# Kernel optimization log

Measured on AMD Instinct MI355X. Metric: run time of the kernel, lower is better.

The kernel has to match this reference:

```python
import jax, jax.numpy as jnp
import numpy as np

NUM_USERS = 100000
NUM_ITEMS = 50000
NUM_OTHERS = 20000
N_NODES = NUM_USERS + NUM_ITEMS + NUM_OTHERS
LATENT_DIM = 64
N_LAYERS = 3
NNZ = 5000000
BATCH = 8192


def setup_inputs() -> dict:
    key = jax.random.key(0)
    ks = jax.random.split(key, 8)
    user_emb = jax.random.normal(ks[0], (NUM_USERS, LATENT_DIM), dtype=jnp.float32) * 0.1
    item_emb = jax.random.normal(ks[1], (NUM_ITEMS, LATENT_DIM), dtype=jnp.float32) * 0.1
    other_emb = jax.random.normal(ks[2], (NUM_OTHERS, LATENT_DIM), dtype=jnp.float32) * 0.1
    # normalized-adjacency-like positive values (symmetric norm values are small positives)
    vals = jax.random.uniform(ks[3], (NNZ,), dtype=jnp.float32) * 0.02
    row_idx = jax.random.randint(ks[4], (NNZ,), 0, N_NODES, dtype=jnp.int64 if jax.config.jax_enable_x64 else jnp.int32)
    col_idx = jax.random.randint(ks[5], (NNZ,), 0, N_NODES, dtype=jnp.int64 if jax.config.jax_enable_x64 else jnp.int32)
    users = jax.random.randint(ks[6], (BATCH,), 0, NUM_USERS, dtype=jnp.int32)
    items = jax.random.randint(ks[7], (BATCH,), 0, NUM_ITEMS, dtype=jnp.int32)
    return {
        "user_emb": user_emb,
        "item_emb": item_emb,
        "other_emb": other_emb,
        "vals": vals,
        "row_idx": row_idx,
        "col_idx": col_idx,
        "users": users,
        "items": items,
    }


def _spmm(vals, row_idx, col_idx, x):
    # sparse.mm(A, x): out[r] = sum_{(r,c) in A} vals * x[c]
    gathered = vals[:, None] * x[col_idx]  # [nnz, d]
    return jax.ops.segment_sum(gathered, row_idx, num_segments=N_NODES)


def reference(user_emb, item_emb, other_emb, vals, row_idx, col_idx, users, items):
    all_emb = jnp.concatenate([user_emb, item_emb, other_emb], axis=0)  # [N, d]
    acc = all_emb
    cur = all_emb
    for _ in range(N_LAYERS):
        cur = _spmm(vals, row_idx, col_idx, cur)
        acc = acc + cur
    lgn_out = acc / jnp.float32(N_LAYERS + 1)  # mean over stacked layer embeddings
    all_users = lgn_out[:NUM_USERS]
    all_items = lgn_out[NUM_USERS:NUM_USERS + NUM_ITEMS]
    users_embs = all_users[users]  # [B, d]
    items_embs = all_items[items]  # [B, d]
    gamma = jnp.sum(users_embs * items_embs, axis=1)  # [B]
    return gamma
```

## Files before the change

### kernel.cpp

```cpp
#include <hip/hip_runtime.h>

#define NUM_USERS 100000
#define NUM_ITEMS 50000
#define NUM_OTHERS 20000
#define N_NODES 170000
#define DIM 64
#define NNZ 5000000
#define BATCH 8192

#define BSHIFT 10
#define RPB (1 << BSHIFT)
#define NBUCK ((N_NODES + RPB - 1) / RPB)
#define COLMASK 0x3FFFF
#define NBLK 512
#define CHUNK ((NNZ + NBLK - 1) / NBLK)
#define HBLK 1024
#define HCHUNK ((NNZ + HBLK - 1) / HBLK)

typedef float f32x2 __attribute__((ext_vector_type(2)));

static __device__ __forceinline__ unsigned f2bf(float f) {
    unsigned u = __float_as_uint(f);
    u = (u + 0x7fff + ((u >> 16) & 1)) >> 16;
    return u;
}
static __device__ __forceinline__ float bflo(unsigned u) {
    return __uint_as_float(u << 16);
}
static __device__ __forceinline__ float bfhi(unsigned u) {
    return __uint_as_float(u & 0xFFFF0000u);
}

__global__ void build_cur0(const float* __restrict__ ue,
                           const float* __restrict__ ie,
                           const float* __restrict__ oe,
                           ushort4* __restrict__ cur) {
    const int total = N_NODES * (DIM / 4);
    for (int i = blockIdx.x * blockDim.x + threadIdx.x; i < total;
         i += gridDim.x * blockDim.x) {
        const int node = i >> 4;
        const int sub  = i & 15;
        const float* src;
        if (node < NUM_USERS)                  src = ue + (size_t)node * DIM;
        else if (node < NUM_USERS + NUM_ITEMS) src = ie + (size_t)(node - NUM_USERS) * DIM;
        else                                   src = oe + (size_t)(node - NUM_USERS - NUM_ITEMS) * DIM;
        const float4 f = reinterpret_cast<const float4*>(src)[sub];
        ushort4 o;
        o.x = (unsigned short)f2bf(f.x); o.y = (unsigned short)f2bf(f.y);
        o.z = (unsigned short)f2bf(f.z); o.w = (unsigned short)f2bf(f.w);
        cur[i] = o;
    }
}

__global__ void init_acc(const int* __restrict__ users,
                         const int* __restrict__ items,
                         const float* __restrict__ ue,
                         const float* __restrict__ ie,
                         float4* __restrict__ uacc,
                         float4* __restrict__ iacc) {
    const int total = BATCH * (DIM / 4);
    int i = blockIdx.x * blockDim.x + threadIdx.x;
    if (i >= total) return;
    const int b = i >> 4;
    const int sub = i & 15;
    uacc[i] = reinterpret_cast<const float4*>(ue + (size_t)users[b] * DIM)[sub];
    iacc[i] = reinterpret_cast<const float4*>(ie + (size_t)items[b] * DIM)[sub];
}

__global__ __launch_bounds__(256) void bucket_hist(const int* __restrict__ rows,
                                                   int* __restrict__ bucket_cnt) {
    __shared__ int h[NBUCK];
    for (int i = threadIdx.x; i < NBUCK; i += 256) h[i] = 0;
    __syncthreads();
    const int s = blockIdx.x * HCHUNK;
    const int e = min(s + HCHUNK, NNZ);
    for (int i = s + threadIdx.x; i < e; i += 256)
        atomicAdd(&h[rows[i] >> BSHIFT], 1);
    __syncthreads();
    for (int i = threadIdx.x; i < NBUCK; i += 256)
        if (h[i]) atomicAdd(&bucket_cnt[i], h[i]);
}

__global__ __launch_bounds__(256) void bucket_scan(const int* __restrict__ bucket_cnt,
                                                   int* __restrict__ bucket_base,
                                                   int* __restrict__ gcursor) {
    __shared__ int lds[256];
    const int t = threadIdx.x;
    const int v = (t < NBUCK) ? bucket_cnt[t] : 0;
    lds[t] = v;
    __syncthreads();
    int acc = v;
    for (int off = 1; off < 256; off <<= 1) {
        const int add = (t >= off) ? lds[t - off] : 0;
        __syncthreads();
        acc += add;
        lds[t] = acc;
        __syncthreads();
    }
    if (t < NBUCK) {
        const int ex = acc - v;
        bucket_base[t] = ex;
        gcursor[t] = ex;
    }
    if (t == 0) bucket_base[NBUCK] = NNZ;
}

__global__ __launch_bounds__(256) void bucket_scatter(const int* __restrict__ rows,
                                                      const int* __restrict__ cols,
                                                      const float* __restrict__ vals,
                                                      int* __restrict__ gcursor,
                                                      int2* __restrict__ bkt) {
    __shared__ int h[NBUCK];
    __shared__ int base[NBUCK];
    for (int i = threadIdx.x; i < NBUCK; i += 256) h[i] = 0;
    __syncthreads();
    const int s = blockIdx.x * CHUNK;
    const int e = min(s + CHUNK, NNZ);
    for (int i = s + threadIdx.x; i < e; i += 256)
        atomicAdd(&h[rows[i] >> BSHIFT], 1);
    __syncthreads();
    for (int i = threadIdx.x; i < NBUCK; i += 256)
        base[i] = h[i] ? atomicAdd(&gcursor[i], h[i]) : 0;
    __syncthreads();
    for (int i = threadIdx.x; i < NBUCK; i += 256) h[i] = 0;
    __syncthreads();
    for (int i = s + threadIdx.x; i < e; i += 256) {
        const int r  = rows[i];
        const int bk = r >> BSHIFT;
        const int lr = r & (RPB - 1);
        const int pos = base[bk] + atomicAdd(&h[bk], 1);
        bkt[pos] = make_int2((lr << 18) | cols[i], __float_as_int(vals[i]));
    }
}

__global__ __launch_bounds__(512) void bucket_to_csr(const int* __restrict__ bucket_base,
                                                     const int2* __restrict__ bkt,
                                                     unsigned* __restrict__ rowinfo,
                                                     int2* __restrict__ packed) {
    __shared__ int cnt[RPB];
    __shared__ int rs[RPB];
    __shared__ int tsum[512];
    const int k = blockIdx.x;
    const int rbase = k << BSHIFT;
    const int bs = bucket_base[k];
    const int be = bucket_base[k + 1];
    const int t = threadIdx.x;

    cnt[t] = 0; cnt[t + 512] = 0;
    __syncthreads();
    for (int i = bs + t; i < be; i += 512)
        atomicAdd(&cnt[bkt[i].x >> 18], 1);
    __syncthreads();

    const int v0 = cnt[2 * t];
    const int v1 = cnt[2 * t + 1];
    int acc = v0 + v1;
    tsum[t] = acc;
    __syncthreads();
    for (int off = 1; off < 512; off <<= 1) {
        const int add = (t >= off) ? tsum[t - off] : 0;
        __syncthreads();
        acc += add;
        tsum[t] = acc;
        __syncthreads();
    }
    const int excl = acc - (v0 + v1);
    rs[2 * t]     = excl;
    rs[2 * t + 1] = excl + v0;
    if (rbase + 2 * t < N_NODES)
        rowinfo[rbase + 2 * t]     = ((unsigned)(bs + excl) << 8) | (unsigned)v0;
    if (rbase + 2 * t + 1 < N_NODES)
        rowinfo[rbase + 2 * t + 1] = ((unsigned)(bs + excl + v0) << 8) | (unsigned)v1;
    __syncthreads();

    for (int i = bs + t; i < be; i += 512) {
        const int2 pk = bkt[i];
        const int lr = pk.x >> 18;
        const int pos = bs + atomicAdd(&rs[lr], 1);
        packed[pos] = make_int2(pk.x & COLMASK, pk.y);
    }
}

static __device__ __forceinline__ void spmm_row_accum(
        const unsigned long long* __restrict__ packed,
        const unsigned short* __restrict__ x,
        int s, int e, int g, int d8,
        f32x2& a0, f32x2& a1, f32x2& a2, f32x2& a3) {
    for (int i = s; i < e; i += 32) {
        const int j0 = i + g;
        const int j1 = j0 + 8;
        const int j2 = j0 + 16;
        const int j3 = j0 + 24;
        const unsigned long long p0 = __builtin_nontemporal_load(packed + j0);
        const unsigned long long p1 = __builtin_nontemporal_load(packed + j1);
        const unsigned long long p2 = __builtin_nontemporal_load(packed + j2);
        const unsigned long long p3 = __builtin_nontemporal_load(packed + j3);
        const int   c0 = (j0 < e) ? (int)(p0 & 0xFFFFFFFFu) : 0;
        const int   c1 = (j1 < e) ? (int)(p1 & 0xFFFFFFFFu) : 0;
        const int   c2 = (j2 < e) ? (int)(p2 & 0xFFFFFFFFu) : 0;
        const int   c3 = (j3 < e) ? (int)(p3 & 0xFFFFFFFFu) : 0;
        const float v0 = (j0 < e) ? __uint_as_float((unsigned)(p0 >> 32)) : 0.f;
        const float v1 = (j1 < e) ? __uint_as_float((unsigned)(p1 >> 32)) : 0.f;
        const float v2 = (j2 < e) ? __uint_as_float((unsigned)(p2 >> 32)) : 0.f;
        const float v3 = (j3 < e) ? __uint_as_float((unsigned)(p3 >> 32)) : 0.f;
        const uint4 x0 = *reinterpret_cast<const uint4*>(x + c0 * DIM + d8);
        const uint4 x1 = *reinterpret_cast<const uint4*>(x + c1 * DIM + d8);
        const uint4 x2 = *reinterpret_cast<const uint4*>(x + c2 * DIM + d8);
        const uint4 x3 = *reinterpret_cast<const uint4*>(x + c3 * DIM + d8);
        const f32x2 w0 = {v0, v0}, w1 = {v1, v1}, w2 = {v2, v2}, w3 = {v3, v3};
        a0 += w0 * (f32x2){bflo(x0.x), bfhi(x0.x)};
        a1 += w0 * (f32x2){bflo(x0.y), bfhi(x0.y)};
        a2 += w0 * (f32x2){bflo(x0.z), bfhi(x0.z)};
        a3 += w0 * (f32x2){bflo(x0.w), bfhi(x0.w)};
        a0 += w1 * (f32x2){bflo(x1.x), bfhi(x1.x)};
        a1 += w1 * (f32x2){bflo(x1.y), bfhi(x1.y)};
        a2 += w1 * (f32x2){bflo(x1.z), bfhi(x1.z)};
        a3 += w1 * (f32x2){bflo(x1.w), bfhi(x1.w)};
        a0 += w2 * (f32x2){bflo(x2.x), bfhi(x2.x)};
        a1 += w2 * (f32x2){bflo(x2.y), bfhi(x2.y)};
        a2 += w2 * (f32x2){bflo(x2.z), bfhi(x2.z)};
        a3 += w2 * (f32x2){bflo(x2.w), bfhi(x2.w)};
        a0 += w3 * (f32x2){bflo(x3.x), bfhi(x3.x)};
        a1 += w3 * (f32x2){bflo(x3.y), bfhi(x3.y)};
        a2 += w3 * (f32x2){bflo(x3.z), bfhi(x3.z)};
        a3 += w3 * (f32x2){bflo(x3.w), bfhi(x3.w)};
    }
}

static __device__ __forceinline__ void butterfly8(f32x2& a0, f32x2& a1,
                                                  f32x2& a2, f32x2& a3) {
    #pragma unroll
    for (int off = 8; off < 64; off <<= 1) {
        a0.x += __shfl_xor(a0.x, off); a0.y += __shfl_xor(a0.y, off);
        a1.x += __shfl_xor(a1.x, off); a1.y += __shfl_xor(a1.y, off);
        a2.x += __shfl_xor(a2.x, off); a2.y += __shfl_xor(a2.y, off);
        a3.x += __shfl_xor(a3.x, off); a3.y += __shfl_xor(a3.y, off);
    }
}

__global__ __launch_bounds__(256) void spmm_csr8(const unsigned* __restrict__ rowinfo,
                                                 const unsigned long long* __restrict__ packed,
                                                 const unsigned short* __restrict__ x,
                                                 unsigned short* __restrict__ y) {
    const int row  = blockIdx.x * 4 + (threadIdx.x >> 6);
    const int lane = threadIdx.x & 63;
    if (row >= N_NODES) return;
    const unsigned info = rowinfo[row];
    const int s = (int)(info >> 8);
    const int e = s + (int)(info & 0xFFu);
    const int g  = lane >> 3;
    const int d8 = (lane & 7) * 8;

    f32x2 a0 = {0, 0}, a1 = {0, 0}, a2 = {0, 0}, a3 = {0, 0};
    spmm_row_accum(packed, x, s, e, g, d8, a0, a1, a2, a3);
    butterfly8(a0, a1, a2, a3);

    if (lane < 8) {
        uint4 o;
        o.x = f2bf(a0.x) | (f2bf(a0.y) << 16);
        o.y = f2bf(a1.x) | (f2bf(a1.y) << 16);
        o.z = f2bf(a2.x) | (f2bf(a2.y) << 16);
        o.w = f2bf(a3.x) | (f2bf(a3.y) << 16);
        *reinterpret_cast<uint4*>(y + row * DIM + lane * 8) = o;
    }
}

__global__ __launch_bounds__(256) void spmm_batch_final8(const unsigned* __restrict__ rowinfo,
                                                         const unsigned long long* __restrict__ packed,
                                                         const unsigned short* __restrict__ x,
                                                         const int* __restrict__ users,
                                                         const int* __restrict__ items,
                                                         float* __restrict__ uacc,
                                                         float* __restrict__ iacc) {
    const int w    = blockIdx.x * 4 + (threadIdx.x >> 6);
    const int lane = threadIdx.x & 63;
    if (w >= 2 * BATCH) return;
    const int b = w >> 1;
    const int isItem = w & 1;
    const int row = isItem ? (NUM_USERS + items[b]) : users[b];
    const unsigned info = rowinfo[row];
    const int s = (int)(info >> 8);
    const int e = s + (int)(info & 0xFFu);
    const int g  = lane >> 3;
    const int d8 = (lane & 7) * 8;

    f32x2 a0 = {0, 0}, a1 = {0, 0}, a2 = {0, 0}, a3 = {0, 0};
    spmm_row_accum(packed, x, s, e, g, d8, a0, a1, a2, a3);
    butterfly8(a0, a1, a2, a3);

    if (lane < 8) {
        float* dst = (isItem ? iacc : uacc) + (size_t)b * DIM + lane * 8;
        float4 q0 = reinterpret_cast<float4*>(dst)[0];
        float4 q1 = reinterpret_cast<float4*>(dst)[1];
        q0.x += a0.x; q0.y += a0.y; q0.z += a1.x; q0.w += a1.y;
        q1.x += a2.x; q1.y += a2.y; q1.z += a3.x; q1.w += a3.y;
        reinterpret_cast<float4*>(dst)[0] = q0;
        reinterpret_cast<float4*>(dst)[1] = q1;
    }
}

__global__ void gather_add(const int* __restrict__ users,
                           const int* __restrict__ items,
                           const unsigned short* __restrict__ y,
                           float4* __restrict__ uacc,
                           float4* __restrict__ iacc) {
    const int total = BATCH * (DIM / 4);
    int i = blockIdx.x * blockDim.x + threadIdx.x;
    if (i >= total) return;
    const int b = i >> 4;
    const int sub = i & 15;
    const int un = users[b];
    const int in = NUM_USERS + items[b];
    float4 a = uacc[i];
    const ushort4 yu = *reinterpret_cast<const ushort4*>(y + (size_t)un * DIM + sub * 4);
    a.x += bflo(yu.x); a.y += bflo(yu.y); a.z += bflo(yu.z); a.w += bflo(yu.w);
    uacc[i] = a;
    float4 c = iacc[i];
    const ushort4 yi = *reinterpret_cast<const ushort4*>(y + (size_t)in * DIM + sub * 4);
    c.x += bflo(yi.x); c.y += bflo(yi.y); c.z += bflo(yi.z); c.w += bflo(yi.w);
    iacc[i] = c;
}

__global__ void dot_out(const float* __restrict__ uacc,
                        const float* __restrict__ iacc,
                        float* __restrict__ gamma) {
    const int b = blockIdx.x * (blockDim.x / 64) + (threadIdx.x / 64);
    const int lane = threadIdx.x & 63;
    if (b >= BATCH) return;
    float p = uacc[b * DIM + lane] * iacc[b * DIM + lane];
    #pragma unroll
    for (int off = 32; off > 0; off >>= 1) p += __shfl_down(p, off);
    if (lane == 0) gamma[b] = p * 0.0625f;
}

extern "C" void kernel_launch(void* const* d_in, const int* in_sizes, int n_in,
                              void* d_out, int out_size, void* d_ws, size_t ws_size,
                              hipStream_t stream) {
    const float* ue    = (const float*)d_in[0];
    const float* ie    = (const float*)d_in[1];
    const float* oe    = (const float*)d_in[2];
    const float* vals  = (const float*)d_in[3];
    const int*   rows  = (const int*)d_in[4];
    const int*   cols  = (const int*)d_in[5];
    const int*   users = (const int*)d_in[6];
    const int*   items = (const int*)d_in[7];
    float* out = (float*)d_out;

    char* p = (char*)d_ws;
    int2* bkt = (int2*)p;
    unsigned short* cur = (unsigned short*)p;
    p += (size_t)NNZ * sizeof(int2);
    unsigned short* nxt = (unsigned short*)p;
    p += (size_t)N_NODES * DIM * sizeof(unsigned short);
    int2* packed = (int2*)p;  p += (size_t)(NNZ + 32) * sizeof(int2);
    unsigned* rowinfo = (unsigned*)p;  p += (size_t)(N_NODES + 4) * sizeof(unsigned);
    int* bucket_cnt  = (int*)p;  p += (size_t)(NBUCK + 4) * sizeof(int);
    int* bucket_base = (int*)p;  p += (size_t)(NBUCK + 4) * sizeof(int);
    int* gcursor     = (int*)p;  p += (size_t)(NBUCK + 4) * sizeof(int);
    float* uacc = (float*)p;  p += (size_t)BATCH * DIM * sizeof(float);
    float* iacc = (float*)p;  p += (size_t)BATCH * DIM * sizeof(float);

    hipMemsetAsync(bucket_cnt, 0, (size_t)NBUCK * sizeof(int), stream);
    bucket_hist<<<HBLK, 256, 0, stream>>>(rows, bucket_cnt);
    bucket_scan<<<1, 256, 0, stream>>>(bucket_cnt, bucket_base, gcursor);
    bucket_scatter<<<NBLK, 256, 0, stream>>>(rows, cols, vals, gcursor, bkt);
    bucket_to_csr<<<NBUCK, 512, 0, stream>>>(bucket_base, bkt, rowinfo, packed);

    build_cur0<<<2048, 256, 0, stream>>>(ue, ie, oe, (ushort4*)cur);
    init_acc<<<(BATCH * 16 + 255) / 256, 256, 0, stream>>>(users, items, ue, ie,
                                                           (float4*)uacc, (float4*)iacc);

    for (int layer = 0; layer < 2; ++layer) {
        spmm_csr8<<<(N_NODES + 3) / 4, 256, 0, stream>>>(rowinfo,
                                                         (const unsigned long long*)packed,
                                                         cur, nxt);
        gather_add<<<(BATCH * 16 + 255) / 256, 256, 0, stream>>>(users, items, nxt,
                                                                 (float4*)uacc, (float4*)iacc);
        unsigned short* t = cur; cur = nxt; nxt = t;
    }

    spmm_batch_final8<<<(2 * BATCH + 3) / 4, 256, 0, stream>>>(rowinfo,
                                                               (const unsigned long long*)packed,
                                                               cur, users, items, uacc, iacc);

    dot_out<<<BATCH / 4, 256, 0, stream>>>(uacc, iacc, out);
}
```

Baseline: 377.1 us.

## Pad CSR rows to multiples of 32 and store pre-scaled byte offsets

The CSR build now pads every row to a multiple of 32 entries with zero-valued dummy entries, using per-bucket slack offsets. The SpMM inner loop can therefore drop all bounds checks and selects. Column indices are stored pre-shifted as byte offsets, which removes a multiply in the gather address. The cost is extra padded entries: with about 29 nonzeros per row, most rows grow to 32 or 64 entries. That means more packed-array traffic and wasted FMAs, plus serial per-thread zero-fill loops in the CSR build.

```diff
diff --git a/kernel.cpp b/kernel.cpp
--- a/kernel.cpp
+++ b/kernel.cpp
@@ -12,6 +12,7 @@
 #define RPB (1 << BSHIFT)
 #define NBUCK ((N_NODES + RPB - 1) / RPB)
 #define COLMASK 0x3FFFF
+#define PADSLACK (31 * RPB)
 #define NBLK 512
 #define CHUNK ((NNZ + NBLK - 1) / NBLK)
 #define HBLK 1024
@@ -83,6 +84,7 @@
 
 __global__ __launch_bounds__(256) void bucket_scan(const int* __restrict__ bucket_cnt,
                                                    int* __restrict__ bucket_base,
+                                                   int* __restrict__ pad_base,
                                                    int* __restrict__ gcursor) {
     __shared__ int lds[256];
     const int t = threadIdx.x;
@@ -101,6 +103,7 @@
         const int ex = acc - v;
         bucket_base[t] = ex;
         gcursor[t] = ex;
+        pad_base[t] = ex + t * PADSLACK;
     }
     if (t == 0) bucket_base[NBUCK] = NNZ;
 }
@@ -134,6 +137,7 @@
 }
 
 __global__ __launch_bounds__(512) void bucket_to_csr(const int* __restrict__ bucket_base,
+                                                     const int* __restrict__ pad_base,
                                                      const int2* __restrict__ bkt,
                                                      unsigned* __restrict__ rowinfo,
                                                      int2* __restrict__ packed) {
@@ -142,8 +146,9 @@
     __shared__ int tsum[512];
     const int k = blockIdx.x;
     const int rbase = k << BSHIFT;
-    const int bs = bucket_base[k];
-    const int be = bucket_base[k + 1];
+    const int bs  = bucket_base[k];
+    const int be  = bucket_base[k + 1];
+    const int pbs = pad_base[k];
     const int t = threadIdx.x;
 
     cnt[t] = 0; cnt[t + 512] = 0;
@@ -154,7 +159,9 @@
 
     const int v0 = cnt[2 * t];
     const int v1 = cnt[2 * t + 1];
-    int acc = v0 + v1;
+    const int pl0 = (v0 + 31) & ~31;
+    const int pl1 = (v1 + 31) & ~31;
+    int acc = pl0 + pl1;
     tsum[t] = acc;
     __syncthreads();
     for (int off = 1; off < 512; off <<= 1) {
@@ -164,49 +171,50 @@
         tsum[t] = acc;
         __syncthreads();
     }
-    const int excl = acc - (v0 + v1);
+    const int excl = acc - (pl0 + pl1);
     rs[2 * t]     = excl;
-    rs[2 * t + 1] = excl + v0;
+    rs[2 * t + 1] = excl + pl0;
     if (rbase + 2 * t < N_NODES)
-        rowinfo[rbase + 2 * t]     = ((unsigned)(bs + excl) << 8) | (unsigned)v0;
+        rowinfo[rbase + 2 * t]     = ((unsigned)(pbs + excl) << 8) | (unsigned)(pl0 >> 5);
     if (rbase + 2 * t + 1 < N_NODES)
-        rowinfo[rbase + 2 * t + 1] = ((unsigned)(bs + excl + v0) << 8) | (unsigned)v1;
-    __syncthreads();
+        rowinfo[rbase + 2 * t + 1] = ((unsigned)(pbs + excl + pl0) << 8) | (unsigned)(pl1 >> 5);
+    __syncthreads();
+
+    for (int j = v0; j < pl0; ++j) packed[pbs + excl + j] = make_int2(0, 0);
+    for (int j = v1; j < pl1; ++j) packed[pbs + excl + pl0 + j] = make_int2(0, 0);
 
     for (int i = bs + t; i < be; i += 512) {
         const int2 pk = bkt[i];
         const int lr = pk.x >> 18;
-        const int pos = bs + atomicAdd(&rs[lr], 1);
-        packed[pos] = make_int2(pk.x & COLMASK, pk.y);
+        const int pos = pbs + atomicAdd(&rs[lr], 1);
+        packed[pos] = make_int2((pk.x & COLMASK) << 7, pk.y);
     }
 }
 
 static __device__ __forceinline__ void spmm_row_accum(
         const unsigned long long* __restrict__ packed,
         const unsigned short* __restrict__ x,
-        int s, int e, int g, int d8,
+        int s, int e, int g, int d8b,
         f32x2& a0, f32x2& a1, f32x2& a2, f32x2& a3) {
+    const char* xb = (const char*)x;
     for (int i = s; i < e; i += 32) {
         const int j0 = i + g;
-        const int j1 = j0 + 8;
-        const int j2 = j0 + 16;
-        const int j3 = j0 + 24;
         const unsigned long long p0 = __builtin_nontemporal_load(packed + j0);
-        const unsigned long long p1 = __builtin_nontemporal_load(packed + j1);
-        const unsigned long long p2 = __builtin_nontemporal_load(packed + j2);
-        const unsigned long long p3 = __builtin_nontemporal_load(packed + j3);
-        const int   c0 = (j0 < e) ? (int)(p0 & 0xFFFFFFFFu) : 0;
-        const int   c1 = (j1 < e) ? (int)(p1 & 0xFFFFFFFFu) : 0;
-        const int   c2 = (j2 < e) ? (int)(p2 & 0xFFFFFFFFu) : 0;
-        const int   c3 = (j3 < e) ? (int)(p3 & 0xFFFFFFFFu) : 0;
-        const float v0 = (j0 < e) ? __uint_as_float((unsigned)(p0 >> 32)) : 0.f;
-        const float v1 = (j1 < e) ? __uint_as_float((unsigned)(p1 >> 32)) : 0.f;
-        const float v2 = (j2 < e) ? __uint_as_float((unsigned)(p2 >> 32)) : 0.f;
-        const float v3 = (j3 < e) ? __uint_as_float((unsigned)(p3 >> 32)) : 0.f;
-        const uint4 x0 = *reinterpret_cast<const uint4*>(x + c0 * DIM + d8);
-        const uint4 x1 = *reinterpret_cast<const uint4*>(x + c1 * DIM + d8);
-        const uint4 x2 = *reinterpret_cast<const uint4*>(x + c2 * DIM + d8);
-        const uint4 x3 = *reinterpret_cast<const uint4*>(x + c3 * DIM + d8);
+        const unsigned long long p1 = __builtin_nontemporal_load(packed + j0 + 8);
+        const unsigned long long p2 = __builtin_nontemporal_load(packed + j0 + 16);
+        const unsigned long long p3 = __builtin_nontemporal_load(packed + j0 + 24);
+        const unsigned c0 = (unsigned)(p0 & 0xFFFFFFFFu) + d8b;
+        const unsigned c1 = (unsigned)(p1 & 0xFFFFFFFFu) + d8b;
+        const unsigned c2 = (unsigned)(p2 & 0xFFFFFFFFu) + d8b;
+        const unsigned c3 = (unsigned)(p3 & 0xFFFFFFFFu) + d8b;
+        const float v0 = __uint_as_float((unsigned)(p0 >> 32));
+        const float v1 = __uint_as_float((unsigned)(p1 >> 32));
+        const float v2 = __uint_as_float((unsigned)(p2 >> 32));
+        const float v3 = __uint_as_float((unsigned)(p3 >> 32));
+        const uint4 x0 = *reinterpret_cast<const uint4*>(xb + c0);
+        const uint4 x1 = *reinterpret_cast<const uint4*>(xb + c1);
+        const uint4 x2 = *reinterpret_cast<const uint4*>(xb + c2);
+        const uint4 x3 = *reinterpret_cast<const uint4*>(xb + c3);
         const f32x2 w0 = {v0, v0}, w1 = {v1, v1}, w2 = {v2, v2}, w3 = {v3, v3};
         a0 += w0 * (f32x2){bflo(x0.x), bfhi(x0.x)};
         a1 += w0 * (f32x2){bflo(x0.y), bfhi(x0.y)};
@@ -247,12 +255,12 @@
     if (row >= N_NODES) return;
     const unsigned info = rowinfo[row];
     const int s = (int)(info >> 8);
-    const int e = s + (int)(info & 0xFFu);
-    const int g  = lane >> 3;
-    const int d8 = (lane & 7) * 8;
+    const int e = s + ((int)(info & 0xFFu) << 5);
+    const int g   = lane >> 3;
+    const int d8b = (lane & 7) * 16;
 
     f32x2 a0 = {0, 0}, a1 = {0, 0}, a2 = {0, 0}, a3 = {0, 0};
-    spmm_row_accum(packed, x, s, e, g, d8, a0, a1, a2, a3);
+    spmm_row_accum(packed, x, s, e, g, d8b, a0, a1, a2, a3);
     butterfly8(a0, a1, a2, a3);
 
     if (lane < 8) {
@@ -280,12 +288,12 @@
     const int row = isItem ? (NUM_USERS + items[b]) : users[b];
     const unsigned info = rowinfo[row];
     const int s = (int)(info >> 8);
-    const int e = s + (int)(info & 0xFFu);
-    const int g  = lane >> 3;
-    const int d8 = (lane & 7) * 8;
+    const int e = s + ((int)(info & 0xFFu) << 5);
+    const int g   = lane >> 3;
+    const int d8b = (lane & 7) * 16;
 
     f32x2 a0 = {0, 0}, a1 = {0, 0}, a2 = {0, 0}, a3 = {0, 0};
-    spmm_row_accum(packed, x, s, e, g, d8, a0, a1, a2, a3);
+    spmm_row_accum(packed, x, s, e, g, d8b, a0, a1, a2, a3);
     butterfly8(a0, a1, a2, a3);
 
     if (lane < 8) {
@@ -352,19 +360,21 @@
     p += (size_t)NNZ * sizeof(int2);
     unsigned short* nxt = (unsigned short*)p;
     p += (size_t)N_NODES * DIM * sizeof(unsigned short);
-    int2* packed = (int2*)p;  p += (size_t)(NNZ + 32) * sizeof(int2);
+    int2* packed = (int2*)p;
+    p += (size_t)(NNZ + (size_t)NBUCK * PADSLACK + 64) * sizeof(int2);
     unsigned* rowinfo = (unsigned*)p;  p += (size_t)(N_NODES + 4) * sizeof(unsigned);
     int* bucket_cnt  = (int*)p;  p += (size_t)(NBUCK + 4) * sizeof(int);
     int* bucket_base = (int*)p;  p += (size_t)(NBUCK + 4) * sizeof(int);
+    int* pad_base    = (int*)p;  p += (size_t)(NBUCK + 4) * sizeof(int);
     int* gcursor     = (int*)p;  p += (size_t)(NBUCK + 4) * sizeof(int);
     float* uacc = (float*)p;  p += (size_t)BATCH * DIM * sizeof(float);
     float* iacc = (float*)p;  p += (size_t)BATCH * DIM * sizeof(float);
 
     hipMemsetAsync(bucket_cnt, 0, (size_t)NBUCK * sizeof(int), stream);
     bucket_hist<<<HBLK, 256, 0, stream>>>(rows, bucket_cnt);
-    bucket_scan<<<1, 256, 0, stream>>>(bucket_cnt, bucket_base, gcursor);
+    bucket_scan<<<1, 256, 0, stream>>>(bucket_cnt, bucket_base, pad_base, gcursor);
     bucket_scatter<<<NBLK, 256, 0, stream>>>(rows, cols, vals, gcursor, bkt);
-    bucket_to_csr<<<NBUCK, 512, 0, stream>>>(bucket_base, bkt, rowinfo, packed);
+    bucket_to_csr<<<NBUCK, 512, 0, stream>>>(bucket_base, pad_base, bkt, rowinfo, packed);
 
     build_cur0<<<2048, 256, 0, stream>>>(ue, ie, oe, (ushort4*)cur);
     init_acc<<<(BATCH * 16 + 255) / 256, 256, 0, stream>>>(users, items, ue, ie,
```

Measured after the change: 401.5 us. 6.5% more time.

## Replace bucket histogram/scan with fixed-capacity buckets and pre-scaled column offsets

Applied to the files above, without the earlier changes.

Drops the separate histogram and scan kernels by giving each row bucket a fixed capacity slot (32K entries), so scatter gets offsets straight from atomic counters and CSR build addresses each bucket at a fixed base. Column indices are stored pre-multiplied by the row byte stride, which removes the multiply in the SpMM gather address computation. This saves two launches and one full pass over row indices. In exchange the workspace grows, and correctness depends on no bucket exceeding the fixed capacity, which holds for uniform random rows (about 30K per bucket) but is a tight margin.

```diff
diff --git a/kernel.cpp b/kernel.cpp
--- a/kernel.cpp
+++ b/kernel.cpp
@@ -12,10 +12,10 @@
 #define RPB (1 << BSHIFT)
 #define NBUCK ((N_NODES + RPB - 1) / RPB)
 #define COLMASK 0x3FFFF
+#define BCAPSHIFT 15
+#define BCAP (1 << BCAPSHIFT)
 #define NBLK 512
 #define CHUNK ((NNZ + NBLK - 1) / NBLK)
-#define HBLK 1024
-#define HCHUNK ((NNZ + HBLK - 1) / HBLK)
 
 typedef float f32x2 __attribute__((ext_vector_type(2)));
 
@@ -67,48 +67,10 @@
     iacc[i] = reinterpret_cast<const float4*>(ie + (size_t)items[b] * DIM)[sub];
 }
 
-__global__ __launch_bounds__(256) void bucket_hist(const int* __restrict__ rows,
-                                                   int* __restrict__ bucket_cnt) {
-    __shared__ int h[NBUCK];
-    for (int i = threadIdx.x; i < NBUCK; i += 256) h[i] = 0;
-    __syncthreads();
-    const int s = blockIdx.x * HCHUNK;
-    const int e = min(s + HCHUNK, NNZ);
-    for (int i = s + threadIdx.x; i < e; i += 256)
-        atomicAdd(&h[rows[i] >> BSHIFT], 1);
-    __syncthreads();
-    for (int i = threadIdx.x; i < NBUCK; i += 256)
-        if (h[i]) atomicAdd(&bucket_cnt[i], h[i]);
-}
-
-__global__ __launch_bounds__(256) void bucket_scan(const int* __restrict__ bucket_cnt,
-                                                   int* __restrict__ bucket_base,
-                                                   int* __restrict__ gcursor) {
-    __shared__ int lds[256];
-    const int t = threadIdx.x;
-    const int v = (t < NBUCK) ? bucket_cnt[t] : 0;
-    lds[t] = v;
-    __syncthreads();
-    int acc = v;
-    for (int off = 1; off < 256; off <<= 1) {
-        const int add = (t >= off) ? lds[t - off] : 0;
-        __syncthreads();
-        acc += add;
-        lds[t] = acc;
-        __syncthreads();
-    }
-    if (t < NBUCK) {
-        const int ex = acc - v;
-        bucket_base[t] = ex;
-        gcursor[t] = ex;
-    }
-    if (t == 0) bucket_base[NBUCK] = NNZ;
-}
-
 __global__ __launch_bounds__(256) void bucket_scatter(const int* __restrict__ rows,
                                                       const int* __restrict__ cols,
                                                       const float* __restrict__ vals,
-                                                      int* __restrict__ gcursor,
+                                                      int* __restrict__ bucket_cnt,
                                                       int2* __restrict__ bkt) {
     __shared__ int h[NBUCK];
     __shared__ int base[NBUCK];
@@ -120,7 +82,7 @@
         atomicAdd(&h[rows[i] >> BSHIFT], 1);
     __syncthreads();
     for (int i = threadIdx.x; i < NBUCK; i += 256)
-        base[i] = h[i] ? atomicAdd(&gcursor[i], h[i]) : 0;
+        base[i] = h[i] ? atomicAdd(&bucket_cnt[i], h[i]) : 0;
     __syncthreads();
     for (int i = threadIdx.x; i < NBUCK; i += 256) h[i] = 0;
     __syncthreads();
@@ -129,11 +91,12 @@
         const int bk = r >> BSHIFT;
         const int lr = r & (RPB - 1);
         const int pos = base[bk] + atomicAdd(&h[bk], 1);
-        bkt[pos] = make_int2((lr << 18) | cols[i], __float_as_int(vals[i]));
-    }
-}
-
-__global__ __launch_bounds__(512) void bucket_to_csr(const int* __restrict__ bucket_base,
+        bkt[((size_t)bk << BCAPSHIFT) + pos] = make_int2((lr << 18) | cols[i],
+                                                         __float_as_int(vals[i]));
+    }
+}
+
+__global__ __launch_bounds__(512) void bucket_to_csr(const int* __restrict__ bucket_cnt,
                                                      const int2* __restrict__ bkt,
                                                      unsigned* __restrict__ rowinfo,
                                                      int2* __restrict__ packed) {
@@ -142,14 +105,16 @@
     __shared__ int tsum[512];
     const int k = blockIdx.x;
     const int rbase = k << BSHIFT;
-    const int bs = bucket_base[k];
-    const int be = bucket_base[k + 1];
+    const int nvalid = min(RPB, N_NODES - rbase);
+    const int n = bucket_cnt[k];
+    const int2* __restrict__ src = bkt + ((size_t)k << BCAPSHIFT);
+    int2* __restrict__ dst = packed + ((size_t)k << BCAPSHIFT);
     const int t = threadIdx.x;
 
     cnt[t] = 0; cnt[t + 512] = 0;
     __syncthreads();
-    for (int i = bs + t; i < be; i += 512)
-        atomicAdd(&cnt[bkt[i].x >> 18], 1);
+    for (int i = t; i < n; i += 512)
+        atomicAdd(&cnt[src[i].x >> 18], 1);
     __syncthreads();
 
     const int v0 = cnt[2 * t];
@@ -167,25 +132,27 @@
     const int excl = acc - (v0 + v1);
     rs[2 * t]     = excl;
     rs[2 * t + 1] = excl + v0;
-    if (rbase + 2 * t < N_NODES)
-        rowinfo[rbase + 2 * t]     = ((unsigned)(bs + excl) << 8) | (unsigned)v0;
-    if (rbase + 2 * t + 1 < N_NODES)
-        rowinfo[rbase + 2 * t + 1] = ((unsigned)(bs + excl + v0) << 8) | (unsigned)v1;
-    __syncthreads();
-
-    for (int i = bs + t; i < be; i += 512) {
-        const int2 pk = bkt[i];
+    const unsigned abs0 = (unsigned)((k << BCAPSHIFT) + excl);
+    if (2 * t < nvalid)
+        rowinfo[rbase + 2 * t]     = (abs0 << 8) | (unsigned)v0;
+    if (2 * t + 1 < nvalid)
+        rowinfo[rbase + 2 * t + 1] = ((abs0 + (unsigned)v0) << 8) | (unsigned)v1;
+    __syncthreads();
+
+    for (int i = t; i < n; i += 512) {
+        const int2 pk = src[i];
         const int lr = pk.x >> 18;
-        const int pos = bs + atomicAdd(&rs[lr], 1);
-        packed[pos] = make_int2(pk.x & COLMASK, pk.y);
+        const int pos = atomicAdd(&rs[lr], 1);
+        dst[pos] = make_int2((pk.x & COLMASK) << 7, pk.y);
     }
 }
 
 static __device__ __forceinline__ void spmm_row_accum(
         const unsigned long long* __restrict__ packed,
         const unsigned short* __restrict__ x,
-        int s, int e, int g, int d8,
+        int s, int e, int g, int d8b,
         f32x2& a0, f32x2& a1, f32x2& a2, f32x2& a3) {
+    const char* xb = (const char*)x;
     for (int i = s; i < e; i += 32) {
         const int j0 = i + g;
         const int j1 = j0 + 8;
@@ -195,18 +162,18 @@
         const unsigned long long p1 = __builtin_nontemporal_load(packed + j1);
         const unsigned long long p2 = __builtin_nontemporal_load(packed + j2);
         const unsigned long long p3 = __builtin_nontemporal_load(packed + j3);
-        const int   c0 = (j0 < e) ? (int)(p0 & 0xFFFFFFFFu) : 0;
-        const int   c1 = (j1 < e) ? (int)(p1 & 0xFFFFFFFFu) : 0;
-        const int   c2 = (j2 < e) ? (int)(p2 & 0xFFFFFFFFu) : 0;
-        const int   c3 = (j3 < e) ? (int)(p3 & 0xFFFFFFFFu) : 0;
+        const unsigned c0 = ((j0 < e) ? (unsigned)(p0 & 0xFFFFFFFFu) : 0u) + d8b;
+        const unsigned c1 = ((j1 < e) ? (unsigned)(p1 & 0xFFFFFFFFu) : 0u) + d8b;
+        const unsigned c2 = ((j2 < e) ? (unsigned)(p2 & 0xFFFFFFFFu) : 0u) + d8b;
+        const unsigned c3 = ((j3 < e) ? (unsigned)(p3 & 0xFFFFFFFFu) : 0u) + d8b;
         const float v0 = (j0 < e) ? __uint_as_float((unsigned)(p0 >> 32)) : 0.f;
         const float v1 = (j1 < e) ? __uint_as_float((unsigned)(p1 >> 32)) : 0.f;
         const float v2 = (j2 < e) ? __uint_as_float((unsigned)(p2 >> 32)) : 0.f;
         const float v3 = (j3 < e) ? __uint_as_float((unsigned)(p3 >> 32)) : 0.f;
-        const uint4 x0 = *reinterpret_cast<const uint4*>(x + c0 * DIM + d8);
-        const uint4 x1 = *reinterpret_cast<const uint4*>(x + c1 * DIM + d8);
-        const uint4 x2 = *reinterpret_cast<const uint4*>(x + c2 * DIM + d8);
-        const uint4 x3 = *reinterpret_cast<const uint4*>(x + c3 * DIM + d8);
+        const uint4 x0 = *reinterpret_cast<const uint4*>(xb + c0);
+        const uint4 x1 = *reinterpret_cast<const uint4*>(xb + c1);
+        const uint4 x2 = *reinterpret_cast<const uint4*>(xb + c2);
+        const uint4 x3 = *reinterpret_cast<const uint4*>(xb + c3);
         const f32x2 w0 = {v0, v0}, w1 = {v1, v1}, w2 = {v2, v2}, w3 = {v3, v3};
         a0 += w0 * (f32x2){bflo(x0.x), bfhi(x0.x)};
         a1 += w0 * (f32x2){bflo(x0.y), bfhi(x0.y)};
@@ -248,11 +215,11 @@
     const unsigned info = rowinfo[row];
     const int s = (int)(info >> 8);
     const int e = s + (int)(info & 0xFFu);
-    const int g  = lane >> 3;
-    const int d8 = (lane & 7) * 8;
+    const int g   = lane >> 3;
+    const int d8b = (lane & 7) * 16;
 
     f32x2 a0 = {0, 0}, a1 = {0, 0}, a2 = {0, 0}, a3 = {0, 0};
-    spmm_row_accum(packed, x, s, e, g, d8, a0, a1, a2, a3);
+    spmm_row_accum(packed, x, s, e, g, d8b, a0, a1, a2, a3);
     butterfly8(a0, a1, a2, a3);
 
     if (lane < 8) {
@@ -261,7 +228,7 @@
         o.y = f2bf(a1.x) | (f2bf(a1.y) << 16);
         o.z = f2bf(a2.x) | (f2bf(a2.y) << 16);
         o.w = f2bf(a3.x) | (f2bf(a3.y) << 16);
-        *reinterpret_cast<uint4*>(y + row * DIM + lane * 8) = o;
+        *reinterpret_cast<uint4*>(y + (size_t)row * DIM + lane * 8) = o;
     }
 }
 
@@ -281,11 +248,11 @@
     const unsigned info = rowinfo[row];
     const int s = (int)(info >> 8);
     const int e = s + (int)(info & 0xFFu);
-    const int g  = lane >> 3;
-    const int d8 = (lane & 7) * 8;
+    const int g   = lane >> 3;
+    const int d8b = (lane & 7) * 16;
 
     f32x2 a0 = {0, 0}, a1 = {0, 0}, a2 = {0, 0}, a3 = {0, 0};
-    spmm_row_accum(packed, x, s, e, g, d8, a0, a1, a2, a3);
+    spmm_row_accum(packed, x, s, e, g, d8b, a0, a1, a2, a3);
     butterfly8(a0, a1, a2, a3);
 
     if (lane < 8) {
@@ -349,22 +316,19 @@
     char* p = (char*)d_ws;
     int2* bkt = (int2*)p;
     unsigned short* cur = (unsigned short*)p;
-    p += (size_t)NNZ * sizeof(int2);
+    p += ((size_t)NBUCK << BCAPSHIFT) * sizeof(int2);
     unsigned short* nxt = (unsigned short*)p;
     p += (size_t)N_NODES * DIM * sizeof(unsigned short);
-    int2* packed = (int2*)p;  p += (size_t)(NNZ + 32) * sizeof(int2);
+    int2* packed = (int2*)p;
+    p += (((size_t)NBUCK << BCAPSHIFT) + 64) * sizeof(int2);
     unsigned* rowinfo = (unsigned*)p;  p += (size_t)(N_NODES + 4) * sizeof(unsigned);
-    int* bucket_cnt  = (int*)p;  p += (size_t)(NBUCK + 4) * sizeof(int);
-    int* bucket_base = (int*)p;  p += (size_t)(NBUCK + 4) * sizeof(int);
-    int* gcursor     = (int*)p;  p += (size_t)(NBUCK + 4) * sizeof(int);
+    int* bucket_cnt = (int*)p;  p += (size_t)(NBUCK + 4) * sizeof(int);
     float* uacc = (float*)p;  p += (size_t)BATCH * DIM * sizeof(float);
     float* iacc = (float*)p;  p += (size_t)BATCH * DIM * sizeof(float);
 
     hipMemsetAsync(bucket_cnt, 0, (size_t)NBUCK * sizeof(int), stream);
-    bucket_hist<<<HBLK, 256, 0, stream>>>(rows, bucket_cnt);
-    bucket_scan<<<1, 256, 0, stream>>>(bucket_cnt, bucket_base, gcursor);
-    bucket_scatter<<<NBLK, 256, 0, stream>>>(rows, cols, vals, gcursor, bkt);
-    bucket_to_csr<<<NBUCK, 512, 0, stream>>>(bucket_base, bkt, rowinfo, packed);
+    bucket_scatter<<<NBLK, 256, 0, stream>>>(rows, cols, vals, bucket_cnt, bkt);
+    bucket_to_csr<<<NBUCK, 512, 0, stream>>>(bucket_cnt, bkt, rowinfo, packed);
 
     build_cur0<<<2048, 256, 0, stream>>>(ue, ie, oe, (ushort4*)cur);
     init_acc<<<(BATCH * 16 + 255) / 256, 256, 0, stream>>>(users, items, ue, ie,
@@ -379,7 +343,7 @@
         unsigned short* t = cur; cur = nxt; nxt = t;
     }
 
-    spmm_batch_final8<<<(2 * BATCH + 3) / 4, 256, 0, stream>>>(rowinfo,
+    spmm_batch_final8<<<(2 * BATCH) / 4 + 1, 256, 0, stream>>>(rowinfo,
                                                                (const unsigned long long*)packed,
                                                                cur, users, items, uacc, iacc);
 
```

After: 341.2 us. 1.11x faster.
